# Kernel optimization log

Hardware: AMD Instinct MI355X
Metric: run time of the kernel (lower is better)

The kernel has to match this reference:

```python
import jax, jax.numpy as jnp
import numpy as np

K = 3        # neighborhood kernel per spatial dim
DIL = 1      # dilation per spatial dim
NH = 8       # num heads
C = 64       # embed dims
EPS = 1e-5   # InstanceNorm eps


def _interp_axis(x, axis, out_len):
    # 1D linear interpolation with align_corners=True semantics
    in_len = x.shape[axis]
    pos = jnp.arange(out_len, dtype=jnp.float32) * ((in_len - 1) / (out_len - 1))
    i0 = jnp.clip(jnp.floor(pos).astype(jnp.int32), 0, in_len - 2)
    w = pos - i0.astype(jnp.float32)
    shape = [1] * x.ndim
    shape[axis] = out_len
    w = w.reshape(shape)
    return jnp.take(x, i0, axis=axis) * (1.0 - w) + jnp.take(x, i0 + 1, axis=axis) * w


def _upsample2_trilinear(x):
    # separable trilinear upsample x2 over the three spatial axes (2,3,4)
    for ax in (2, 3, 4):
        x = _interp_axis(x, ax, 2 * x.shape[ax])
    return x


def _instance_norm(t):
    # InstanceNorm3d, affine=False: normalize per (B,C) over spatial dims
    m = jnp.mean(t, axis=(2, 3, 4), keepdims=True)
    v = jnp.var(t, axis=(2, 3, 4), keepdims=True)
    return (t - m) * jax.lax.rsqrt(v + EPS)


def _nbr_idx(L, k, d):
    # NATTEN-style clamped neighborhood: window shifts to stay in-bounds at edges
    i = np.arange(L)
    start = np.clip(i - d * (k // 2), 0, L - d * (k - 1) - 1)
    idx = start[:, None] + np.arange(k)[None, :] * d          # (L,k) absolute nbr index
    rel = (idx - i[:, None]) // d + (k - 1)                   # (L,k) rel-pos-bias index in [0,2k-2]
    return jnp.asarray(idx), jnp.asarray(rel)


def _nca3d(qs, kv, Wq, bq, Wk, bk, Wv, bv, Wo, bo, rpb):
    # qs, kv: (B,H,W,Z,C) channels-last; q from skip, k/v from upsampled x
    B, H, W, Z, Cc = qs.shape
    dh = Cc // NH
    scale = dh ** -0.5
    q = (qs @ Wq + bq).reshape(B, H, W, Z, NH, dh) * scale
    k = (kv @ Wk + bk).reshape(B, H, W, Z, NH, dh)
    v = (kv @ Wv + bv).reshape(B, H, W, Z, NH, dh)

    ih, rh = _nbr_idx(H, K, DIL)
    iw, rw = _nbr_idx(W, K, DIL)
    iz, rz = _nbr_idx(Z, K, DIL)

    def gather_nbrs(t):
        t = jnp.take(t, ih, axis=1)   # (B,H,k,W,Z,nh,dh)
        t = jnp.take(t, iw, axis=3)   # (B,H,k,W,k,Z,nh,dh)
        t = jnp.take(t, iz, axis=5)   # (B,H,k,W,k,Z,k,nh,dh)
        t = jnp.transpose(t, (0, 1, 3, 5, 7, 2, 4, 6, 8))
        return t.reshape(B, H, W, Z, NH, K * K * K, dh)

    kg = gather_nbrs(k)
    vg = gather_nbrs(v)

    logits = jnp.einsum('bxyzhd,bxyzhmd->bxyzhm', q, kg)  # (B,H,W,Z,nh,27)

    # relative position bias: rpb (nh, 2k-1, 2k-1, 2k-1) gathered per query position
    bias = rpb[:, rh]                    # (nh,H,k,2k-1,2k-1)
    bias = jnp.take(bias, rw, axis=3)    # (nh,H,k,W,k,2k-1)
    bias = jnp.take(bias, rz, axis=5)    # (nh,H,k,W,k,Z,k)
    bias = jnp.transpose(bias, (1, 3, 5, 0, 2, 4, 6)).reshape(H, W, Z, NH, K * K * K)

    attn = jax.nn.softmax(logits + bias, axis=-1)
    o = jnp.einsum('bxyzhm,bxyzhmd->bxyzhd', attn, vg).reshape(B, H, W, Z, Cc)
    o = o @ Wo + bo
    return jnp.transpose(o, (0, 4, 1, 2, 3))  # back to (B,C,H,W,Z)


def setup_inputs() -> dict:
    key = jax.random.key(0)
    ks = jax.random.split(key, 8)
    s = 1.0 / np.sqrt(C)
    inp = {
        'x': jax.random.normal(ks[0], (1, C, 32, 32, 8), dtype=jnp.float32),
        'skip': jax.random.normal(ks[1], (1, C, 64, 64, 16), dtype=jnp.float32),
        'Wq': jax.random.normal(ks[2], (C, C), dtype=jnp.float32) * s,
        'bq': jnp.zeros((C,), dtype=jnp.float32),
        'Wk': jax.random.normal(ks[3], (C, C), dtype=jnp.float32) * s,
        'bk': jnp.zeros((C,), dtype=jnp.float32),
        'Wv': jax.random.normal(ks[4], (C, C), dtype=jnp.float32) * s,
        'bv': jnp.zeros((C,), dtype=jnp.float32),
        'Wo': jax.random.normal(ks[5], (C, C), dtype=jnp.float32) * s,
        'bo': jnp.zeros((C,), dtype=jnp.float32),
        'rpb': jax.random.normal(ks[6], (NH, 2 * K - 1, 2 * K - 1, 2 * K - 1), dtype=jnp.float32) * 0.02,
    }
    return inp


def reference(x, skip, Wq, bq, Wk, bk, Wv, bv, Wo, bo, rpb):
    xu = _instance_norm(_upsample2_trilinear(x))   # (B,C,2H,2W,2Z) == skip shape
    sk = _instance_norm(skip)
    qs = jnp.transpose(sk, (0, 2, 3, 4, 1))        # queries from skip
    kv = jnp.transpose(xu, (0, 2, 3, 4, 1))        # keys/values from upsampled x
    return _nca3d(qs, kv, Wq, bq, Wk, bk, Wv, bv, Wo, bo, rpb)
```

## Files before the change

### kernel.cpp

```cpp
#include <hip/hip_runtime.h>
#include <hip/hip_bf16.h>

typedef __hip_bfloat16 bf16;
typedef __attribute__((ext_vector_type(8))) short short8;
typedef __attribute__((ext_vector_type(4))) float f32x4;

static constexpr int NPOS = 65536;

__device__ __forceinline__ float bs2f(short s) {
  union { float f; unsigned u; } cv;
  cv.u = ((unsigned)(unsigned short)s) << 16;
  return cv.f;
}
__device__ __forceinline__ short f2bs(float f) {
  bf16 b = __float2bfloat16(f);
  short r;
  __builtin_memcpy(&r, &b, 2);
  return r;
}

__global__ __launch_bounds__(256) void k_partial(const float* __restrict__ x,
                                                 const float* __restrict__ skip,
                                                 bf16* __restrict__ xu,
                                                 float* __restrict__ partials) {
  __shared__ float s1[256];
  __shared__ float s2[256];
  int b = blockIdx.x, tid = threadIdx.x;
  float sum = 0.f, sq = 0.f;
  if (b < 1024) {
    int c = b >> 4;
    int h = (b & 15) * 4 + (tid >> 6);
    int w = tid & 63;
    float fh = (float)h * (31.0f / 63.0f);
    int ih = (int)fh; if (ih > 30) ih = 30;
    float wh = fh - (float)ih;
    float fw = (float)w * (31.0f / 63.0f);
    int iw = (int)fw; if (iw > 30) iw = 30;
    float ww = fw - (float)iw;
    const float* base = x + c * 8192 + ih * 256 + iw * 8;
    float4 A0 = *(const float4*)(base);
    float4 A1 = *(const float4*)(base + 4);
    float4 B0 = *(const float4*)(base + 8);
    float4 B1 = *(const float4*)(base + 12);
    float4 C0 = *(const float4*)(base + 256);
    float4 C1 = *(const float4*)(base + 260);
    float4 D0 = *(const float4*)(base + 264);
    float4 D1 = *(const float4*)(base + 268);
    float ra[8] = {A0.x, A0.y, A0.z, A0.w, A1.x, A1.y, A1.z, A1.w};
    float rb[8] = {B0.x, B0.y, B0.z, B0.w, B1.x, B1.y, B1.z, B1.w};
    float rc[8] = {C0.x, C0.y, C0.z, C0.w, C1.x, C1.y, C1.z, C1.w};
    float rd[8] = {D0.x, D0.y, D0.z, D0.w, D1.x, D1.y, D1.z, D1.w};
    short8 o0, o1;
#pragma unroll
    for (int z = 0; z < 16; z++) {
      float fz = (float)z * (7.0f / 15.0f);
      int iz = (int)fz; if (iz > 6) iz = 6;
      float wz = fz - (float)iz;
      float va = ra[iz] * (1.f - wz) + ra[iz + 1] * wz;
      float vb = rb[iz] * (1.f - wz) + rb[iz + 1] * wz;
      float vc = rc[iz] * (1.f - wz) + rc[iz + 1] * wz;
      float vd = rd[iz] * (1.f - wz) + rd[iz + 1] * wz;
      float v0 = va * (1.f - ww) + vb * ww;
      float v1 = vc * (1.f - ww) + vd * ww;
      float v = v0 * (1.f - wh) + v1 * wh;
      sum += v; sq += v * v;
      if (z < 8) o0[z] = f2bs(v); else o1[z - 8] = f2bs(v);
    }
    bf16* xo = xu + (size_t)c * NPOS + h * 1024 + w * 16;
    *(short8*)xo = o0;
    *(short8*)(xo + 8) = o1;
  } else {
    int bb = b - 1024;
    const float4* p =
        (const float4*)(skip + (size_t)(bb >> 4) * NPOS + (bb & 15) * 4096);
    for (int i = tid; i < 1024; i += 256) {
      float4 v = p[i];
      sum += v.x + v.y + v.z + v.w;
      sq += v.x * v.x + v.y * v.y + v.z * v.z + v.w * v.w;
    }
  }
  s1[tid] = sum; s2[tid] = sq;
  __syncthreads();
  for (int s = 128; s > 0; s >>= 1) {
    if (tid < s) { s1[tid] += s1[tid + s]; s2[tid] += s2[tid + s]; }
    __syncthreads();
  }
  if (tid == 0) { partials[2 * b] = s1[0]; partials[2 * b + 1] = s2[0]; }
}

__global__ __launch_bounds__(256) void k_proj_mfma(
    const bf16* __restrict__ xu, const float* __restrict__ skip,
    const float* __restrict__ partials,
    const float* __restrict__ Wk, const float* __restrict__ bk,
    const float* __restrict__ Wv, const float* __restrict__ bv,
    const float* __restrict__ Wq, const float* __restrict__ bq,
    bf16* __restrict__ kbuf, bf16* __restrict__ vbuf, bf16* __restrict__ qbuf) {
  __shared__ float stl[256];
  __shared__ short xa[64 * 72];
  __shared__ short wb[64 * 72];
  __shared__ short ob[64 * 72];
  int tid = threadIdx.x;
  int p0 = blockIdx.x * 64;

  if (tid < 128) {
    int isk = tid >> 6, c = tid & 63;
    int base = isk ? (1024 + c * 16) : (c * 16);
    float sum = 0.f, sq = 0.f;
#pragma unroll
    for (int j = 0; j < 16; j++) {
      sum += partials[2 * (base + j)];
      sq  += partials[2 * (base + j) + 1];
    }
    float m = sum * (1.0f / NPOS);
    float var = sq * (1.0f / NPOS) - m * m;
    stl[isk * 128 + c] = m;
    stl[isk * 128 + 64 + c] = rsqrtf(var + 1e-5f);
  }
  __syncthreads();

  for (int ii = tid; ii < 512; ii += 256) {
    int c = ii >> 3, t0 = (ii & 7) * 8;
    short8 v8 = *(const short8*)(xu + (size_t)c * NPOS + p0 + t0);
    float m = stl[c], r = stl[64 + c];
#pragma unroll
    for (int u = 0; u < 8; u++) xa[(t0 + u) * 72 + c] = f2bs((bs2f(v8[u]) - m) * r);
  }
  {
    int c = tid >> 2, j0 = (tid & 3) * 16;
    const float4* wr = (const float4*)(Wk + c * 64 + j0);
    float4 w0 = wr[0], w1 = wr[1], w2 = wr[2], w3 = wr[3];
    float wv[16] = {w0.x,w0.y,w0.z,w0.w, w1.x,w1.y,w1.z,w1.w,
                    w2.x,w2.y,w2.z,w2.w, w3.x,w3.y,w3.z,w3.w};
#pragma unroll
    for (int u = 0; u < 16; u++) wb[(j0 + u) * 72 + c] = f2bs(wv[u]);
  }
  __syncthreads();

  int wv_ = tid >> 6, lane = tid & 63, quad = lane >> 4, l15 = lane & 15;
  const short* arow = &xa[(wv_ * 16 + l15) * 72 + quad * 8];
  int orow0 = (wv_ * 16 + quad * 4);

  {
    short8 a0 = *(const short8*)(arow);
    short8 a1 = *(const short8*)(arow + 32);
#pragma unroll
    for (int nt = 0; nt < 4; nt++) {
      const short* brow = &wb[(nt * 16 + l15) * 72 + quad * 8];
      short8 b0 = *(const short8*)(brow);
      short8 b1 = *(const short8*)(brow + 32);
      f32x4 acc = {0.f, 0.f, 0.f, 0.f};
      acc = __builtin_amdgcn_mfma_f32_16x16x32_bf16(a0, b0, acc, 0, 0, 0);
      acc = __builtin_amdgcn_mfma_f32_16x16x32_bf16(a1, b1, acc, 0, 0, 0);
      float bval = bk[nt * 16 + l15];
#pragma unroll
      for (int r = 0; r < 4; r++)
        ob[(orow0 + r) * 72 + nt * 16 + l15] = f2bs(acc[r] + bval);
    }
  }
  __syncthreads();
  {
    int row = tid >> 2, col0 = (tid & 3) * 16;
    short8 o0 = *(const short8*)(&ob[row * 72 + col0]);
    short8 o1 = *(const short8*)(&ob[row * 72 + col0 + 8]);
    *(short8*)(kbuf + (size_t)(p0 + row) * 64 + col0) = o0;
    *(short8*)(kbuf + (size_t)(p0 + row) * 64 + col0 + 8) = o1;
    int c = tid >> 2, j0 = (tid & 3) * 16;
    const float4* wr = (const float4*)(Wv + c * 64 + j0);
    float4 w0 = wr[0], w1 = wr[1], w2 = wr[2], w3 = wr[3];
    float wvv[16] = {w0.x,w0.y,w0.z,w0.w, w1.x,w1.y,w1.z,w1.w,
                     w2.x,w2.y,w2.z,w2.w, w3.x,w3.y,w3.z,w3.w};
#pragma unroll
    for (int u = 0; u < 16; u++) wb[(j0 + u) * 72 + c] = f2bs(wvv[u]);
  }
  __syncthreads();
  {
    short8 a0 = *(const short8*)(arow);
    short8 a1 = *(const short8*)(arow + 32);
#pragma unroll
    for (int nt = 0; nt < 4; nt++) {
      const short* brow = &wb[(nt * 16 + l15) * 72 + quad * 8];
      short8 b0 = *(const short8*)(brow);
      short8 b1 = *(const short8*)(brow + 32);
      f32x4 acc = {0.f, 0.f, 0.f, 0.f};
      acc = __builtin_amdgcn_mfma_f32_16x16x32_bf16(a0, b0, acc, 0, 0, 0);
      acc = __builtin_amdgcn_mfma_f32_16x16x32_bf16(a1, b1, acc, 0, 0, 0);
      float bval = bv[nt * 16 + l15];
#pragma unroll
      for (int r = 0; r < 4; r++)
        ob[(orow0 + r) * 72 + nt * 16 + l15] = f2bs(acc[r] + bval);
    }
  }
  __syncthreads();
  {
    int row = tid >> 2, col0 = (tid & 3) * 16;
    short8 o0 = *(const short8*)(&ob[row * 72 + col0]);
    short8 o1 = *(const short8*)(&ob[row * 72 + col0 + 8]);
    *(short8*)(vbuf + (size_t)(p0 + row) * 64 + col0) = o0;
    *(short8*)(vbuf + (size_t)(p0 + row) * 64 + col0 + 8) = o1;
  }
  for (int ii = tid; ii < 1024; ii += 256) {
    int c = ii >> 4, t0 = (ii & 15) * 4;
    float4 v = *(const float4*)(skip + (size_t)c * NPOS + p0 + t0);
    float m = stl[128 + c], r = stl[192 + c];
    xa[(t0 + 0) * 72 + c] = f2bs((v.x - m) * r);
    xa[(t0 + 1) * 72 + c] = f2bs((v.y - m) * r);
    xa[(t0 + 2) * 72 + c] = f2bs((v.z - m) * r);
    xa[(t0 + 3) * 72 + c] = f2bs((v.w - m) * r);
  }
  {
    int c = tid >> 2, j0 = (tid & 3) * 16;
    const float4* wr = (const float4*)(Wq + c * 64 + j0);
    float4 w0 = wr[0], w1 = wr[1], w2 = wr[2], w3 = wr[3];
    float wq_[16] = {w0.x,w0.y,w0.z,w0.w, w1.x,w1.y,w1.z,w1.w,
                     w2.x,w2.y,w2.z,w2.w, w3.x,w3.y,w3.z,w3.w};
#pragma unroll
    for (int u = 0; u < 16; u++) wb[(j0 + u) * 72 + c] = f2bs(wq_[u]);
  }
  __syncthreads();
  {
    const float scale = 0.35355339059327373f;
    short8 a0 = *(const short8*)(arow);
    short8 a1 = *(const short8*)(arow + 32);
#pragma unroll
    for (int nt = 0; nt < 4; nt++) {
      const short* brow = &wb[(nt * 16 + l15) * 72 + quad * 8];
      short8 b0 = *(const short8*)(brow);
      short8 b1 = *(const short8*)(brow + 32);
      f32x4 acc = {0.f, 0.f, 0.f, 0.f};
      acc = __builtin_amdgcn_mfma_f32_16x16x32_bf16(a0, b0, acc, 0, 0, 0);
      acc = __builtin_amdgcn_mfma_f32_16x16x32_bf16(a1, b1, acc, 0, 0, 0);
      float bval = bq[nt * 16 + l15];
#pragma unroll
      for (int r = 0; r < 4; r++)
        ob[(orow0 + r) * 72 + nt * 16 + l15] = f2bs((acc[r] + bval) * scale);
    }
  }
  __syncthreads();
  {
    int row = tid >> 2, col0 = (tid & 3) * 16;
    short8 o0 = *(const short8*)(&ob[row * 72 + col0]);
    short8 o1 = *(const short8*)(&ob[row * 72 + col0 + 8]);
    *(short8*)(qbuf + (size_t)(p0 + row) * 64 + col0) = o0;
    *(short8*)(qbuf + (size_t)(p0 + row) * 64 + col0 + 8) = o1;
  }
}

__global__ __launch_bounds__(512, 2) void k_attn(
    const bf16* __restrict__ qbuf, const bf16* __restrict__ kbuf,
    const bf16* __restrict__ vbuf,
    const float* __restrict__ Wo, const float* __restrict__ bo,
    const float* __restrict__ rpb, float* __restrict__ out) {
  __shared__ float rp[1000];
  __shared__ float oT[64 * 65];
  int tid = threadIdx.x;
  int b = blockIdx.x;
  int sb = ((b & 7) << 7) + (b >> 3);
  int p0 = sb * 64;
  for (int i = tid; i < 1000; i += 512) rp[i] = rpb[i];
  __syncthreads();

  int head = tid & 7, pp = tid >> 3;
  int p = p0 + pp;
  int h = p >> 10, w = (p >> 4) & 63, z = p & 15;

  short8 q8 = *(const short8*)(qbuf + (size_t)p * 64 + head * 8);
  float q[8];
#pragma unroll
  for (int d = 0; d < 8; d++) q[d] = bs2f(q8[d]);

  int sh = h - 1; if (sh < 0) sh = 0; if (sh > 61) sh = 61;
  int sw = w - 1; if (sw < 0) sw = 0; if (sw > 61) sw = 61;
  int sz = z - 1; if (sz < 0) sz = 0; if (sz > 13) sz = 13;

  const bf16* kb = kbuf + (size_t)(sh * 1024 + sw * 16 + sz) * 64 + head * 8;
  const bf16* vb = vbuf + (size_t)(sh * 1024 + sw * 16 + sz) * 64 + head * 8;
  int rbase = ((sh - h + 2) * 5 + (sw - w + 2)) * 5 + (sz - z + 2) + head * 125;

  float s[27];
#pragma unroll
  for (int j = 0; j < 27; j++) {
    int kh = j / 9, kw = (j % 9) / 3, kz = j % 3;
    int coff = (kh * 1024 + kw * 16 + kz) * 64;
    short8 k8 = *(const short8*)(kb + coff);
    float sv = q[0] * bs2f(k8[0]) + q[1] * bs2f(k8[1]) +
               q[2] * bs2f(k8[2]) + q[3] * bs2f(k8[3]) +
               q[4] * bs2f(k8[4]) + q[5] * bs2f(k8[5]) +
               q[6] * bs2f(k8[6]) + q[7] * bs2f(k8[7]);
    s[j] = sv + rp[rbase + (kh * 5 + kw) * 5 + kz];
  }
  float M = s[26];
#pragma unroll
  for (int j = 0; j < 13; j++) M = fmaxf(M, fmaxf(s[2 * j], s[2 * j + 1]));

  float lrun = 0.f;
  float oa[8];
#pragma unroll
  for (int d = 0; d < 8; d++) oa[d] = 0.f;
#pragma unroll
  for (int j = 0; j < 27; j++) {
    int kh = j / 9, kw = (j % 9) / 3, kz = j % 3;
    int coff = (kh * 1024 + kw * 16 + kz) * 64;
    short8 v8 = *(const short8*)(vb + coff);
    float pw = __expf(s[j] - M);
    lrun += pw;
#pragma unroll
    for (int d = 0; d < 8; d++) oa[d] += pw * bs2f(v8[d]);
  }
  float inv = 1.0f / lrun;
#pragma unroll
  for (int d = 0; d < 8; d++) oT[pp * 65 + head * 8 + d] = oa[d] * inv;
  __syncthreads();

  int wid = __builtin_amdgcn_readfirstlane(tid >> 6);
  int l = tid & 63;
  float acc[8];
#pragma unroll
  for (int u = 0; u < 8; u++) acc[u] = bo[wid * 8 + u];
  for (int j = 0; j < 64; j++) {
    float ov = oT[l * 65 + j];
    const float* wr = Wo + j * 64 + wid * 8;
#pragma unroll
    for (int u = 0; u < 8; u++) acc[u] += ov * wr[u];
  }
#pragma unroll
  for (int u = 0; u < 8; u++)
    out[(size_t)(wid * 8 + u) * NPOS + p0 + l] = acc[u];
}

extern "C" void kernel_launch(void* const* d_in, const int* in_sizes, int n_in,
                              void* d_out, int out_size, void* d_ws, size_t ws_size,
                              hipStream_t stream) {
  const float* x    = (const float*)d_in[0];
  const float* skip = (const float*)d_in[1];
  const float* Wq   = (const float*)d_in[2];
  const float* bq   = (const float*)d_in[3];
  const float* Wk   = (const float*)d_in[4];
  const float* bk   = (const float*)d_in[5];
  const float* Wv   = (const float*)d_in[6];
  const float* bv   = (const float*)d_in[7];
  const float* Wo   = (const float*)d_in[8];
  const float* bo   = (const float*)d_in[9];
  const float* rpb  = (const float*)d_in[10];

  bf16* xu        = (bf16*)d_ws;
  bf16* kbuf      = (bf16*)((char*)d_ws + ((size_t)8 << 20));
  bf16* vbuf      = (bf16*)((char*)d_ws + ((size_t)16 << 20));
  bf16* qbuf      = (bf16*)((char*)d_ws + ((size_t)24 << 20));
  float* partials = (float*)((char*)d_ws + ((size_t)32 << 20));
  float* out = (float*)d_out;

  hipLaunchKernelGGL(k_partial, dim3(2048), dim3(256), 0, stream, x, skip, xu,
                     partials);
  hipLaunchKernelGGL(k_proj_mfma, dim3(1024), dim3(256), 0, stream, xu, skip,
                     partials, Wk, bk, Wv, bv, Wq, bq, kbuf, vbuf, qbuf);
  hipLaunchKernelGGL(k_attn, dim3(1024), dim3(512), 0, stream, qbuf, kbuf, vbuf,
                     Wo, bo, rpb, out);
}
```

Before: 147.5 us.

## Split attention neighbours across two thread teams and stage Wo in shared memory

The attention kernel now uses two threads per (position, head), each covering about half of the 27 neighbours, with a duplicated middle slot masked in one team. The max, sum and output accumulators are combined with cross-lane shuffles. Blocks shrink to 16 positions and 256 threads with a 4x larger grid, and the output projection reads Wo from shared memory instead of global. The upsample z-loop also gets compile-time interpolation indices via a macro. This costs more blocks, a per-block copy of Wo into shared memory, and shuffle overhead in exchange for fewer registers per thread and more parallelism.

```diff
diff --git a/kernel.cpp b/kernel.cpp
--- a/kernel.cpp
+++ b/kernel.cpp
@@ -51,21 +51,25 @@
     float rc[8] = {C0.x, C0.y, C0.z, C0.w, C1.x, C1.y, C1.z, C1.w};
     float rd[8] = {D0.x, D0.y, D0.z, D0.w, D1.x, D1.y, D1.z, D1.w};
     short8 o0, o1;
-#pragma unroll
-    for (int z = 0; z < 16; z++) {
-      float fz = (float)z * (7.0f / 15.0f);
-      int iz = (int)fz; if (iz > 6) iz = 6;
-      float wz = fz - (float)iz;
-      float va = ra[iz] * (1.f - wz) + ra[iz + 1] * wz;
-      float vb = rb[iz] * (1.f - wz) + rb[iz + 1] * wz;
-      float vc = rc[iz] * (1.f - wz) + rc[iz + 1] * wz;
-      float vd = rd[iz] * (1.f - wz) + rd[iz + 1] * wz;
-      float v0 = va * (1.f - ww) + vb * ww;
-      float v1 = vc * (1.f - ww) + vd * ww;
-      float v = v0 * (1.f - wh) + v1 * wh;
-      sum += v; sq += v * v;
-      if (z < 8) o0[z] = f2bs(v); else o1[z - 8] = f2bs(v);
-    }
+#define ZSTEP(zz)                                                              \
+  {                                                                            \
+    constexpr float fz = (float)(zz) * (7.0f / 15.0f);                         \
+    constexpr int izr = (int)fz;                                               \
+    constexpr int iz = (izr > 6) ? 6 : izr;                                    \
+    constexpr float wz = fz - (float)iz;                                       \
+    float va = ra[iz] * (1.f - wz) + ra[iz + 1] * wz;                          \
+    float vb = rb[iz] * (1.f - wz) + rb[iz + 1] * wz;                          \
+    float vc = rc[iz] * (1.f - wz) + rc[iz + 1] * wz;                          \
+    float vd = rd[iz] * (1.f - wz) + rd[iz + 1] * wz;                          \
+    float v0 = va * (1.f - ww) + vb * ww;                                      \
+    float v1 = vc * (1.f - ww) + vd * ww;                                      \
+    float v = v0 * (1.f - wh) + v1 * wh;                                       \
+    sum += v; sq += v * v;                                                     \
+    if ((zz) < 8) o0[(zz) & 7] = f2bs(v); else o1[(zz) & 7] = f2bs(v);         \
+  }
+    ZSTEP(0) ZSTEP(1) ZSTEP(2) ZSTEP(3) ZSTEP(4) ZSTEP(5) ZSTEP(6) ZSTEP(7)
+    ZSTEP(8) ZSTEP(9) ZSTEP(10) ZSTEP(11) ZSTEP(12) ZSTEP(13) ZSTEP(14) ZSTEP(15)
+#undef ZSTEP
     bf16* xo = xu + (size_t)c * NPOS + h * 1024 + w * 16;
     *(short8*)xo = o0;
     *(short8*)(xo + 8) = o1;
@@ -245,21 +249,24 @@
   }
 }
 
-__global__ __launch_bounds__(512, 2) void k_attn(
+__global__ __launch_bounds__(256, 5) void k_attn(
     const bf16* __restrict__ qbuf, const bf16* __restrict__ kbuf,
     const bf16* __restrict__ vbuf,
     const float* __restrict__ Wo, const float* __restrict__ bo,
     const float* __restrict__ rpb, float* __restrict__ out) {
   __shared__ float rp[1000];
-  __shared__ float oT[64 * 65];
+  __shared__ float wo[4096];
+  __shared__ float oT[16 * 65];
   int tid = threadIdx.x;
   int b = blockIdx.x;
-  int sb = ((b & 7) << 7) + (b >> 3);
-  int p0 = sb * 64;
-  for (int i = tid; i < 1000; i += 512) rp[i] = rpb[i];
-  __syncthreads();
-
-  int head = tid & 7, pp = tid >> 3;
+  int sb = ((b & 7) << 9) + (b >> 3);
+  int p0 = sb * 16;
+  for (int i = tid; i < 1000; i += 256) rp[i] = rpb[i];
+  for (int i = tid; i < 1024; i += 256)
+    ((float4*)wo)[i] = ((const float4*)Wo)[i];
+  __syncthreads();
+
+  int head = tid & 7, team = (tid >> 3) & 1, pp = tid >> 4;
   int p = p0 + pp;
   int h = p >> 10, w = (p >> 4) & 63, z = p & 15;
 
@@ -276,55 +283,69 @@
   const bf16* vb = vbuf + (size_t)(sh * 1024 + sw * 16 + sz) * 64 + head * 8;
   int rbase = ((sh - h + 2) * 5 + (sw - w + 2)) * 5 + (sz - z + 2) + head * 125;
 
-  float s[27];
-#pragma unroll
-  for (int j = 0; j < 27; j++) {
-    int kh = j / 9, kw = (j % 9) / 3, kz = j % 3;
-    int coff = (kh * 1024 + kw * 16 + kz) * 64;
+  static constexpr int CJ0[14] = {0, 64, 128, 1024, 1088, 1152, 2048, 2112,
+                                  2176, 65536, 65600, 65664, 66560, 66624};
+  static constexpr int CJ1[14] = {66624, 66688, 67584, 67648, 67712, 131072,
+                                  131136, 131200, 132096, 132160, 132224,
+                                  133120, 133184, 133248};
+  static constexpr int RJ0[14] = {0, 1, 2, 5, 6, 7, 10, 11, 12, 25, 26, 27, 30, 31};
+  static constexpr int RJ1[14] = {31, 32, 35, 36, 37, 50, 51, 52, 55, 56, 57,
+                                  60, 61, 62};
+
+  float s[14];
+#pragma unroll
+  for (int jj = 0; jj < 14; jj++) {
+    int coff = team ? CJ1[jj] : CJ0[jj];
+    int roff = team ? RJ1[jj] : RJ0[jj];
     short8 k8 = *(const short8*)(kb + coff);
     float sv = q[0] * bs2f(k8[0]) + q[1] * bs2f(k8[1]) +
                q[2] * bs2f(k8[2]) + q[3] * bs2f(k8[3]) +
                q[4] * bs2f(k8[4]) + q[5] * bs2f(k8[5]) +
                q[6] * bs2f(k8[6]) + q[7] * bs2f(k8[7]);
-    s[j] = sv + rp[rbase + (kh * 5 + kw) * 5 + kz];
-  }
-  float M = s[26];
-#pragma unroll
-  for (int j = 0; j < 13; j++) M = fmaxf(M, fmaxf(s[2 * j], s[2 * j + 1]));
+    s[jj] = sv + rp[rbase + roff];
+  }
+  if (team) s[0] = -1e30f;
+
+  float M = fmaxf(s[12], s[13]);
+#pragma unroll
+  for (int j = 0; j < 6; j++) M = fmaxf(M, fmaxf(s[2 * j], s[2 * j + 1]));
+  M = fmaxf(M, __shfl_xor(M, 8, 64));
 
   float lrun = 0.f;
   float oa[8];
 #pragma unroll
   for (int d = 0; d < 8; d++) oa[d] = 0.f;
 #pragma unroll
-  for (int j = 0; j < 27; j++) {
-    int kh = j / 9, kw = (j % 9) / 3, kz = j % 3;
-    int coff = (kh * 1024 + kw * 16 + kz) * 64;
+  for (int jj = 0; jj < 14; jj++) {
+    int coff = team ? CJ1[jj] : CJ0[jj];
     short8 v8 = *(const short8*)(vb + coff);
-    float pw = __expf(s[j] - M);
+    float pw = __expf(s[jj] - M);
     lrun += pw;
 #pragma unroll
     for (int d = 0; d < 8; d++) oa[d] += pw * bs2f(v8[d]);
   }
+  lrun += __shfl_xor(lrun, 8, 64);
+#pragma unroll
+  for (int d = 0; d < 8; d++) oa[d] += __shfl_xor(oa[d], 8, 64);
   float inv = 1.0f / lrun;
-#pragma unroll
-  for (int d = 0; d < 8; d++) oT[pp * 65 + head * 8 + d] = oa[d] * inv;
-  __syncthreads();
-
-  int wid = __builtin_amdgcn_readfirstlane(tid >> 6);
-  int l = tid & 63;
-  float acc[8];
-#pragma unroll
-  for (int u = 0; u < 8; u++) acc[u] = bo[wid * 8 + u];
+  if (team == 0) {
+#pragma unroll
+    for (int d = 0; d < 8; d++) oT[pp * 65 + head * 8 + d] = oa[d] * inv;
+  }
+  __syncthreads();
+
+  int pos = tid & 15, chg = tid >> 4, ch0 = chg * 4;
+  float4 bo4 = *(const float4*)(bo + ch0);
+  float a0 = bo4.x, a1 = bo4.y, a2 = bo4.z, a3 = bo4.w;
   for (int j = 0; j < 64; j++) {
-    float ov = oT[l * 65 + j];
-    const float* wr = Wo + j * 64 + wid * 8;
-#pragma unroll
-    for (int u = 0; u < 8; u++) acc[u] += ov * wr[u];
-  }
-#pragma unroll
-  for (int u = 0; u < 8; u++)
-    out[(size_t)(wid * 8 + u) * NPOS + p0 + l] = acc[u];
+    float ov = oT[pos * 65 + j];
+    float4 wv = *(const float4*)(&wo[j * 64 + ch0]);
+    a0 += ov * wv.x; a1 += ov * wv.y; a2 += ov * wv.z; a3 += ov * wv.w;
+  }
+  out[(size_t)(ch0 + 0) * NPOS + p0 + pos] = a0;
+  out[(size_t)(ch0 + 1) * NPOS + p0 + pos] = a1;
+  out[(size_t)(ch0 + 2) * NPOS + p0 + pos] = a2;
+  out[(size_t)(ch0 + 3) * NPOS + p0 + pos] = a3;
 }
 
 extern "C" void kernel_launch(void* const* d_in, const int* in_sizes, int n_in,
@@ -353,6 +374,6 @@
                      partials);
   hipLaunchKernelGGL(k_proj_mfma, dim3(1024), dim3(256), 0, stream, xu, skip,
                      partials, Wk, bk, Wv, bv, Wq, bq, kbuf, vbuf, qbuf);
-  hipLaunchKernelGGL(k_attn, dim3(1024), dim3(512), 0, stream, qbuf, kbuf, vbuf,
+  hipLaunchKernelGGL(k_attn, dim3(4096), dim3(256), 0, stream, qbuf, kbuf, vbuf,
                      Wo, bo, rpb, out);
 }
```

Measured after the change: 205.3 us. +39.1%, slower.
